# Performance work log

Hardware: AMD Instinct MI355X
Metric: run time of the kernel (lower is better)

## Reference

```python
import jax, jax.numpy as jnp
import numpy as np

B, S, D = 2, 2048, 2048
H, KVH = 32, 8
HD = D // H          # 64
Q_OUT = H * HD       # 2048
KV_OUT = KVH * HD    # 512
THETA = 10000.0


def setup_inputs() -> dict:
    key = jax.random.key(0)
    k1, k2, k3 = jax.random.split(key, 3)
    x = jax.random.normal(k1, (B, S, D), dtype=jnp.float32)
    w_qkv = jax.random.normal(k2, (Q_OUT + 2 * KV_OUT, D), dtype=jnp.float32) * 0.02
    w_out = jax.random.normal(k3, (D, D), dtype=jnp.float32) * 0.02
    gain = jnp.ones((1,), dtype=jnp.float32)
    return {"x": x, "w_qkv": w_qkv, "w_out": w_out, "gain": gain}


def _rope(t):
    # t: [b, s, h, hd]; non-interleaved (half-split) RoPE, positions = arange(s)
    s, hd = t.shape[1], t.shape[-1]
    inv_freq = 1.0 / (THETA ** (jnp.arange(0, hd // 2, dtype=jnp.float32) * 2.0 / hd))
    ang = jnp.arange(s, dtype=jnp.float32)[:, None] * inv_freq[None, :]  # [s, hd/2]
    cos = jnp.cos(ang)[None, :, None, :]
    sin = jnp.sin(ang)[None, :, None, :]
    t1, t2 = t[..., : hd // 2], t[..., hd // 2 :]
    return jnp.concatenate([t1 * cos - t2 * sin, t2 * cos + t1 * sin], axis=-1)


def _rmsnorm(t, eps=1e-6):
    # per-head-dim RMS normalization in fp32 (QK-norm)
    inv = jax.lax.rsqrt(jnp.mean(t * t, axis=-1, keepdims=True) + eps)
    return t * inv


def reference(x, w_qkv, w_out, gain):
    proj = jnp.einsum("bsd,od->bso", x, w_qkv)
    Q = proj[..., :Q_OUT].reshape(B, S, H, HD)
    K = proj[..., Q_OUT : Q_OUT + KV_OUT].reshape(B, S, KVH, HD)
    V = proj[..., Q_OUT + KV_OUT :].reshape(B, S, KVH, HD)

    Q = _rope(Q)
    K = _rope(K)

    # GQA: repeat_interleave kv heads to match query heads
    rep = H // KVH
    K = jnp.repeat(K, rep, axis=2)  # [b, s, H, hd]
    V = jnp.repeat(V, rep, axis=2)

    # value residual path (disabled): alpha1=1, alpha2=0, scale=1 -> V * rsqrt(1 + 1e-8)
    V = V * jax.lax.rsqrt(jnp.float32(1.0 + 1e-8))

    # QK-RMSNorm with learnable scalar gain on q
    Qn = _rmsnorm(Q) * gain
    Kn = _rmsnorm(K)

    scale = 1.0 / jnp.sqrt(jnp.float32(HD))
    scores = jnp.einsum("bqhd,bkhd->bhqk", Qn, Kn) * scale  # [b, H, S, S]
    causal = jnp.tril(jnp.ones((S, S), dtype=bool))
    scores = jnp.where(causal[None, None], scores, jnp.float32(-1e30))
    p = jax.nn.softmax(scores, axis=-1)
    attn = jnp.einsum("bhqk,bkhd->bqhd", p, V)  # [b, S, H, hd]

    # rearrange '(h b) seq hd -> b seq (h hd)': head index is outer in feature dim
    attn_cat = attn.transpose(0, 1, 2, 3).reshape(B, S, H * HD)
    attn_out = jnp.einsum("bsd,od->bso", attn_cat, w_out)

    # module returns (attn_out, V) with V in (h*b, seq, hd) layout
    V_flat = V.transpose(2, 0, 1, 3).reshape(H * B, S, HD)
    return attn_out, V_flat
```

## Files before the change

### kernel.cpp

```cpp
#include <hip/hip_runtime.h>
#include <hip/hip_bf16.h>
#include <cstdint>
#include <cstddef>

#define B_ 2
#define S_ 2048
#define D_ 2048
#define H_ 32
#define KVH_ 8
#define HD_ 64
#define PROJN 3072

typedef unsigned short u16;
typedef unsigned int u32;
typedef __attribute__((ext_vector_type(8))) short short8;
typedef __attribute__((ext_vector_type(4))) short short4v;
typedef __attribute__((ext_vector_type(4))) float f32x4;

__device__ __forceinline__ u16 f2bf(float f) {
  __hip_bfloat16 h = __float2bfloat16(f);
  return *reinterpret_cast<u16*>(&h);
}

__device__ __forceinline__ float fast_exp2(float x) {
  float r;
  asm("v_exp_f32 %0, %1" : "=v"(r) : "v"(x));
  return r;
}

__device__ __forceinline__ u32 pack2bf(float lo, float hi) {
  u32 a = __float_as_uint(lo) + 0x8000u;
  u32 b = __float_as_uint(hi) + 0x8000u;
  return __builtin_amdgcn_perm(b, a, 0x07060302);
}

#define GLDS16(g, l)                                                           \
  __builtin_amdgcn_global_load_lds(                                            \
      (const __attribute__((address_space(1))) void*)(g),                      \
      (__attribute__((address_space(3))) void*)(l), 16, 0, 0)

__global__ __launch_bounds__(256) void pack_bf16(const float* __restrict__ in,
                                                 u16* __restrict__ out, int n) {
  int i = (blockIdx.x * 256 + threadIdx.x) * 8;
  if (i >= n) return;
  const float4* p = reinterpret_cast<const float4*>(in + i);
  float4 a = p[0], b = p[1];
  union { short8 v; u16 u[8]; } r;
  r.u[0] = f2bf(a.x); r.u[1] = f2bf(a.y); r.u[2] = f2bf(a.z); r.u[3] = f2bf(a.w);
  r.u[4] = f2bf(b.x); r.u[5] = f2bf(b.y); r.u[6] = f2bf(b.z); r.u[7] = f2bf(b.w);
  *reinterpret_cast<short8*>(out + i) = r.v;
}

__global__ __launch_bounds__(256) void rope_tabT(float* __restrict__ tct,
                                                 float* __restrict__ tst) {
  int i = blockIdx.x * 256 + threadIdx.x;
  int j = i >> 11, s = i & 2047;
  float e = (float)(2 * j) / 64.0f;
  float inv_freq = 1.0f / powf(10000.0f, e);
  float ang = (float)s * inv_freq;
  tct[i] = cosf(ang);
  tst[i] = sinf(ang);
}

__global__ __launch_bounds__(512) void gemm_bt(const u16* __restrict__ A,
                                               const u16* __restrict__ Bw,
                                               float* __restrict__ C, int M,
                                               int N, int K) {
  __shared__ u16 As[128 * 64];
  __shared__ u16 Bs[128 * 64];
  const int tid = threadIdx.x;
  const int lane = tid & 63;
  const int wave = tid >> 6;
  const int ntile = N >> 7;
  const int m0 = (blockIdx.x / ntile) << 7;
  const int n0 = (blockIdx.x % ntile) << 7;
  const int wr = (wave >> 1) << 5;
  const int wc = (wave & 1) << 6;
  const int arow = lane & 15;
  const int kgrp = lane >> 4;

  const f32x4 zero4 = {0.f, 0.f, 0.f, 0.f};
  f32x4 acc[2][4];
#pragma unroll
  for (int m = 0; m < 2; m++)
#pragma unroll
    for (int n = 0; n < 4; n++) acc[m][n] = zero4;

  int srow[2], sslot[2];
#pragma unroll
  for (int i = 0; i < 2; i++) {
    int c = i * 512 + tid;
    srow[i] = c >> 3;
    sslot[i] = (c & 7) ^ (srow[i] & 7);
  }

  auto stage = [&](int kt) {
    const int k0 = kt << 6;
#pragma unroll
    for (int i = 0; i < 2; i++) {
      const u16* ga = A + (size_t)(m0 + srow[i]) * K + k0 + sslot[i] * 8;
      GLDS16(ga, As + (i * 512 + tid) * 8);
    }
#pragma unroll
    for (int i = 0; i < 2; i++) {
      const u16* gb = Bw + (size_t)(n0 + srow[i]) * K + k0 + sslot[i] * 8;
      GLDS16(gb, Bs + (i * 512 + tid) * 8);
    }
  };

  const int KT = K >> 6;
  stage(0);
  for (int kt = 0;; kt++) {
    __syncthreads();
#pragma unroll
    for (int ks = 0; ks < 2; ks++) {
      const int sd = ks * 4 + kgrp;
      short8 a[2], b[4];
#pragma unroll
      for (int m = 0; m < 2; m++) {
        int r = wr + m * 16 + arow;
        a[m] = *reinterpret_cast<const short8*>(As + r * 64 + ((sd ^ (r & 7)) << 3));
      }
#pragma unroll
      for (int n = 0; n < 4; n++) {
        int r = wc + n * 16 + arow;
        b[n] = *reinterpret_cast<const short8*>(Bs + r * 64 + ((sd ^ (r & 7)) << 3));
      }
#pragma unroll
      for (int m = 0; m < 2; m++)
#pragma unroll
        for (int n = 0; n < 4; n++)
          acc[m][n] = __builtin_amdgcn_mfma_f32_16x16x32_bf16(a[m], b[n], acc[m][n], 0, 0, 0);
    }
    if (kt + 1 == KT) break;
    __syncthreads();
    stage(kt + 1);
  }

  const int crow = kgrp * 4;
#pragma unroll
  for (int m = 0; m < 2; m++) {
#pragma unroll
    for (int n = 0; n < 4; n++) {
      float* cp = C + (size_t)(m0 + wr + m * 16 + crow) * N + n0 + wc + n * 16 + arow;
#pragma unroll
      for (int r = 0; r < 4; r++) cp[(size_t)r * N] = acc[m][n][r];
    }
  }
}

__global__ __launch_bounds__(512) void gemm_qkv(
    const u16* __restrict__ A, const u16* __restrict__ Bw,
    const float* __restrict__ tct, const float* __restrict__ tst,
    const float* __restrict__ gain, float* __restrict__ projV,
    u16* __restrict__ Qn, u16* __restrict__ Kn) {
  __shared__ u16 As[128 * 64];
  __shared__ u16 Bs[128 * 64];
  const int tid = threadIdx.x;
  const int lane = tid & 63;
  const int wave = tid >> 6;
  const int ntile = PROJN >> 7;
  const int m0 = (blockIdx.x / ntile) << 7;
  const int n0 = (blockIdx.x % ntile) << 7;
  const int wr = (wave >> 1) << 5;
  const int wc = (wave & 1) << 6;
  const int ql = lane & 15;
  const int g = lane >> 4;
  const int K = 2048;

  const f32x4 zero4 = {0.f, 0.f, 0.f, 0.f};
  f32x4 acc[2][4];
#pragma unroll
  for (int m = 0; m < 2; m++)
#pragma unroll
    for (int n = 0; n < 4; n++) acc[m][n] = zero4;

  int srow[2], sslot[2];
#pragma unroll
  for (int i = 0; i < 2; i++) {
    int c = i * 512 + tid;
    srow[i] = c >> 3;
    sslot[i] = (c & 7) ^ (srow[i] & 7);
  }

  auto stage = [&](int kt) {
    const int k0 = kt << 6;
#pragma unroll
    for (int i = 0; i < 2; i++) {
      const u16* ga = A + (size_t)(m0 + srow[i]) * K + k0 + sslot[i] * 8;
      GLDS16(ga, As + (i * 512 + tid) * 8);
    }
#pragma unroll
    for (int i = 0; i < 2; i++) {
      const u16* gb = Bw + (size_t)(n0 + srow[i]) * K + k0 + sslot[i] * 8;
      GLDS16(gb, Bs + (i * 512 + tid) * 8);
    }
  };

  stage(0);
  for (int kt = 0;; kt++) {
    __syncthreads();
#pragma unroll
    for (int ks = 0; ks < 2; ks++) {
      const int sd = ks * 4 + g;
      short8 a[2], b[4];
#pragma unroll
      for (int m = 0; m < 2; m++) {
        int r = wr + m * 16 + ql;
        a[m] = *reinterpret_cast<const short8*>(As + r * 64 + ((sd ^ (r & 7)) << 3));
      }
#pragma unroll
      for (int n = 0; n < 4; n++) {
        int r = wc + n * 16 + ql;
        b[n] = *reinterpret_cast<const short8*>(Bs + r * 64 + ((sd ^ (r & 7)) << 3));
      }
#pragma unroll
      for (int m = 0; m < 2; m++)
#pragma unroll
        for (int n = 0; n < 4; n++)
          acc[m][n] = __builtin_amdgcn_mfma_f32_16x16x32_bf16(a[m], b[n], acc[m][n], 0, 0, 0);
    }
    if (kt + 1 == 32) break;
    __syncthreads();
    stage(kt + 1);
  }

  const int hslice = (n0 + wc) >> 6;
  const int browbase = m0 + wr + 4 * g;
  const int bb = (m0 + wr) >> 11;

  if (hslice >= 40) {
    float* dstV = projV + (size_t)browbase * 512 + (hslice - 40) * 64;
#pragma unroll
    for (int m = 0; m < 2; m++)
#pragma unroll
      for (int n = 0; n < 4; n++) {
        float* dp = dstV + (size_t)(16 * m) * 512 + n * 16 + ql;
#pragma unroll
        for (int r = 0; r < 4; r++) dp[(size_t)r * 512] = acc[m][n][r];
      }
    return;
  }

  const bool isQ = (hslice < 32);
  const float scale = isQ ? gain[0] * 0.18033688011112042f : 1.0f;
  u16* outp = isQ ? Qn + ((size_t)(bb * H_ + hslice)) * S_ * HD_
                  : Kn + ((size_t)(bb * KVH_ + (hslice - 32))) * S_ * HD_;
  const int jj0 = ql, jj1 = 16 + ql;

#pragma unroll
  for (int m = 0; m < 2; m++) {
    const int sb = (browbase + 16 * m) & (S_ - 1);
    float c0a[4], c1a[4], s0a[4], s1a[4];
    *reinterpret_cast<float4*>(c0a) = *reinterpret_cast<const float4*>(&tct[jj0 * 2048 + sb]);
    *reinterpret_cast<float4*>(c1a) = *reinterpret_cast<const float4*>(&tct[jj1 * 2048 + sb]);
    *reinterpret_cast<float4*>(s0a) = *reinterpret_cast<const float4*>(&tst[jj0 * 2048 + sb]);
    *reinterpret_cast<float4*>(s1a) = *reinterpret_cast<const float4*>(&tst[jj1 * 2048 + sb]);
    float o[4][4], iv[4];
#pragma unroll
    for (int r = 0; r < 4; r++) {
      const float a0 = acc[m][0][r], a1 = acc[m][1][r];
      const float a2 = acc[m][2][r], a3 = acc[m][3][r];
      const float l0 = a0 * c0a[r] - a2 * s0a[r];
      const float l1 = a1 * c1a[r] - a3 * s1a[r];
      const float h0 = a2 * c0a[r] + a0 * s0a[r];
      const float h1 = a3 * c1a[r] + a1 * s1a[r];
      o[0][r] = l0; o[1][r] = l1; o[2][r] = h0; o[3][r] = h1;
      float sr = (l0 * l0 + l1 * l1) + (h0 * h0 + h1 * h1);
      sr += __shfl_xor(sr, 1);
      sr += __shfl_xor(sr, 2);
      sr += __shfl_xor(sr, 4);
      sr += __shfl_xor(sr, 8);
      iv[r] = rsqrtf(sr * (1.0f / 64.0f) + 1e-6f) * scale;
    }
#pragma unroll
    for (int n = 0; n < 4; n++) {
      const int d = n * 16 + ql;
#pragma unroll
      for (int r = 0; r < 4; r++)
        outp[(size_t)(sb + r) * HD_ + d] = f2bf(o[n][r] * iv[r]);
    }
  }
}

__global__ __launch_bounds__(256) void vtrans(const float* __restrict__ projV,
                                              u16* __restrict__ Vt,
                                              float* __restrict__ Vout) {
  __shared__ float tile[64][65];
  const int bid = blockIdx.x;
  const int st = bid & 31;
  const int s0 = st << 6;
  const int kvh = (bid >> 5) & 7;
  const int b = bid >> 8;
  const int t = threadIdx.x;
  const int sr = t >> 2;
  const int d0 = (t & 3) << 4;
  const float* src = projV + ((size_t)(b * S_ + s0 + sr)) * 512 + kvh * 64 + d0;
  float v[16];
#pragma unroll
  for (int i = 0; i < 16; i += 4) {
    float4 x = *reinterpret_cast<const float4*>(src + i);
    v[i] = x.x; v[i + 1] = x.y; v[i + 2] = x.z; v[i + 3] = x.w;
  }
#pragma unroll
  for (int hh = 0; hh < 4; hh++) {
    int hq = kvh * 4 + hh;
    float* dst = Vout + (((size_t)(hq * B_ + b)) * S_ + s0 + sr) * HD_ + d0;
#pragma unroll
    for (int i = 0; i < 16; i += 4)
      *reinterpret_cast<float4*>(dst + i) = make_float4(v[i], v[i + 1], v[i + 2], v[i + 3]);
  }
#pragma unroll
  for (int i = 0; i < 16; i++) tile[sr][d0 + i] = v[i];
  __syncthreads();
  const int d = t >> 2;
  const int sc = (t & 3) << 4;
  union { short8 v8; u16 u[8]; } o0, o1;
#pragma unroll
  for (int i = 0; i < 8; i++) o0.u[i] = f2bf(tile[sc + i][d]);
#pragma unroll
  for (int i = 0; i < 8; i++) o1.u[i] = f2bf(tile[sc + 8 + i][d]);
  u16* dst = Vt + (((size_t)(b * KVH_ + kvh)) * HD_ + d) * S_ + s0 + sc;
  *reinterpret_cast<short8*>(dst) = o0.v8;
  *reinterpret_cast<short8*>(dst + 8) = o1.v8;
}

__global__ __launch_bounds__(256, 2) void attn_fwd(const u16* __restrict__ Qn,
                                                   const u16* __restrict__ Kn,
                                                   const u16* __restrict__ Vt,
                                                   u16* __restrict__ Aout) {
  __shared__ u16 Ks[2][64 * 64];
  __shared__ u16 Vs[2][64 * 64];
  __shared__ u16 Ps[4][1024];
  const int bid = blockIdx.x;
  const int grp = bid & 15;
  const int i = bid >> 4;
  const int qt = 63 - i;
  const int b = grp >> 3;
  const int kvh = grp & 7;
  const int q0 = qt << 5;
  const int JT = (qt >> 1) + 1;
  const int tid = threadIdx.x;
  const int lane = tid & 63;
  const int wave = tid >> 6;
  const int h = kvh * 4 + wave;
  const int ql = lane & 15;
  const int g = lane >> 4;

  short8 qa[2][2];
  int rowq[2];
#pragma unroll
  for (int f = 0; f < 2; f++) {
    rowq[f] = q0 + 16 * f + ql;
    const u16* qb = Qn + (((size_t)(b * H_ + h)) * S_ + rowq[f]) * HD_;
    qa[f][0] = *reinterpret_cast<const short8*>(qb + g * 8);
    qa[f][1] = *reinterpret_cast<const short8*>(qb + 32 + g * 8);
  }

  const f32x4 zero4 = {0.f, 0.f, 0.f, 0.f};
  f32x4 oacc[4][2];
#pragma unroll
  for (int dn = 0; dn < 4; dn++)
#pragma unroll
    for (int f = 0; f < 2; f++) oacc[dn][f] = zero4;
  float psum[2] = {0.f, 0.f};

  const u16* kg = Kn + ((size_t)(b * KVH_ + kvh)) * S_ * HD_;
  const u16* vg = Vt + ((size_t)(b * KVH_ + kvh)) * HD_ * S_;

  const int c0 = tid, c1 = 256 + tid;
  const int r0 = c0 >> 3, sl0 = (c0 & 7) ^ (r0 & 7);
  const int r1 = c1 >> 3, sl1 = (c1 & 7) ^ (r1 & 7);
  const int xsw2 = (ql & 7) << 2;

  auto stage = [&](int jt, int buf) {
    const int j0 = jt << 6;
    GLDS16(kg + (size_t)(j0 + r0) * HD_ + sl0 * 8, Ks[buf] + c0 * 8);
    GLDS16(kg + (size_t)(j0 + r1) * HD_ + sl1 * 8, Ks[buf] + c1 * 8);
    GLDS16(vg + (size_t)r0 * S_ + j0 + sl0 * 8, Vs[buf] + c0 * 8);
    GLDS16(vg + (size_t)r1 * S_ + j0 + sl1 * 8, Vs[buf] + c1 * 8);
  };

  stage(0, 0);
  __syncthreads();
  int cur = 0;
  for (int jt = 0; jt < JT; jt++) {
    if (jt + 1 < JT) stage(jt + 1, cur ^ 1);
    const int j0 = jt << 6;
    const u16* ksb = Ks[cur];
    const u16* vsb = Vs[cur];
    const bool diag = (jt == JT - 1);

    f32x4 sc[4][2];
#pragma unroll
    for (int n = 0; n < 4; n++)
#pragma unroll
      for (int f = 0; f < 2; f++) sc[n][f] = zero4;
    __builtin_amdgcn_s_setprio(1);
#pragma unroll
    for (int ks = 0; ks < 2; ks++) {
      const int sd = ks * 4 + g;
#pragma unroll
      for (int n = 0; n < 4; n++) {
        const int r = n * 16 + ql;
        short8 kf = *reinterpret_cast<const short8*>(ksb + r * 64 + ((sd ^ (r & 7)) << 3));
        sc[n][0] = __builtin_amdgcn_mfma_f32_16x16x32_bf16(kf, qa[0][ks], sc[n][0], 0, 0, 0);
        sc[n][1] = __builtin_amdgcn_mfma_f32_16x16x32_bf16(kf, qa[1][ks], sc[n][1], 0, 0, 0);
      }
    }
    __builtin_amdgcn_s_setprio(0);

    short8 pa[2][2];
#pragma unroll
    for (int f = 0; f < 2; f++) {
      float pv[4][4];
#pragma unroll
      for (int n = 0; n < 4; n++)
#pragma unroll
        for (int r = 0; r < 4; r++)
          pv[n][r] = fast_exp2(sc[n][f][r]);
      if (diag) {
#pragma unroll
        for (int n = 0; n < 4; n++)
#pragma unroll
          for (int r = 0; r < 4; r++)
            if ((j0 + n * 16 + 4 * g + r) > rowq[f]) pv[n][r] = 0.f;
      }
      u32* pw32 = reinterpret_cast<u32*>(Ps[wave]);
#pragma unroll
      for (int n = 0; n < 4; n++) {
        psum[f] += (pv[n][0] + pv[n][1]) + (pv[n][2] + pv[n][3]);
        const int idx = ql * 32 + (((n << 3) + (g << 1)) ^ xsw2);
        pw32[idx] = pack2bf(pv[n][0], pv[n][1]);
        pw32[idx + 1] = pack2bf(pv[n][2], pv[n][3]);
      }
#pragma unroll
      for (int ks = 0; ks < 2; ks++)
        pa[f][ks] = *reinterpret_cast<const short8*>(
            Ps[wave] + ql * 64 + ((32 * ks + 8 * g) ^ (xsw2 << 1)));
    }

    __builtin_amdgcn_s_setprio(1);
#pragma unroll
    for (int ks = 0; ks < 2; ks++) {
      const int sd = ks * 4 + g;
#pragma unroll
      for (int dn = 0; dn < 4; dn++) {
        const int vr = dn * 16 + ql;
        short8 vf = *reinterpret_cast<const short8*>(vsb + vr * 64 + ((sd ^ (vr & 7)) << 3));
        oacc[dn][0] = __builtin_amdgcn_mfma_f32_16x16x32_bf16(vf, pa[0][ks], oacc[dn][0], 0, 0, 0);
        oacc[dn][1] = __builtin_amdgcn_mfma_f32_16x16x32_bf16(vf, pa[1][ks], oacc[dn][1], 0, 0, 0);
      }
    }
    __builtin_amdgcn_s_setprio(0);

    __syncthreads();
    cur ^= 1;
  }

#pragma unroll
  for (int f = 0; f < 2; f++) {
    float s = psum[f];
    s += __shfl_xor(s, 16);
    s += __shfl_xor(s, 32);
    const float il = 1.0f / s;
#pragma unroll
    for (int dn = 0; dn < 4; dn++) {
      union { short4v v; u16 uu[4]; } o;
#pragma unroll
      for (int r = 0; r < 4; r++) o.uu[r] = f2bf(oacc[dn][f][r] * il);
      u16* dst = Aout + ((size_t)b * S_ + rowq[f]) * D_ + h * HD_ + dn * 16 + 4 * g;
      *reinterpret_cast<short4v*>(dst) = o.v;
    }
  }
}

extern "C" void kernel_launch(void* const* d_in, const int* in_sizes, int n_in,
                              void* d_out, int out_size, void* d_ws,
                              size_t ws_size, hipStream_t stream) {
  const float* x = (const float*)d_in[0];
  const float* wqkv = (const float*)d_in[1];
  const float* wout = (const float*)d_in[2];
  const float* gain = (const float*)d_in[3];

  float* out_attn = (float*)d_out;
  float* out_vflat = out_attn + (size_t)B_ * S_ * D_;

  uint8_t* w = (uint8_t*)d_ws;
  u16* xb      = (u16*)(w);
  u16* wqkvb   = (u16*)(w + 16777216);
  u16* woutb   = (u16*)(w + 29360128);
  float* projV = (float*)(w + 37748736);
  u16* Qn      = (u16*)(w + 46137344);
  u16* Kn      = (u16*)(w + 62914560);
  u16* Vt      = (u16*)(w + 67108864);
  u16* attnb   = (u16*)(w + 71303168);
  float* tct   = (float*)(w + 88080384);
  float* tst   = (float*)(w + 88342528);

  pack_bf16<<<4096, 256, 0, stream>>>(x, xb, B_ * S_ * D_);
  pack_bf16<<<3072, 256, 0, stream>>>(wqkv, wqkvb, PROJN * D_);
  pack_bf16<<<2048, 256, 0, stream>>>(wout, woutb, D_ * D_);
  rope_tabT<<<256, 256, 0, stream>>>(tct, tst);

  gemm_qkv<<<(4096 / 128) * (3072 / 128), 512, 0, stream>>>(
      xb, wqkvb, tct, tst, gain, projV, Qn, Kn);
  vtrans<<<B_ * KVH_ * (S_ / 64), 256, 0, stream>>>(projV, Vt, out_vflat);
  attn_fwd<<<B_ * KVH_ * (S_ / 32), 256, 0, stream>>>(Qn, Kn, Vt, attnb);
  gemm_bt<<<(4096 / 128) * (2048 / 128), 512, 0, stream>>>(attnb, woutb,
                                                           out_attn, 4096,
                                                           2048, 2048);
}
```

Measured before the change: 210.1 us.

## Double-buffer LDS in both GEMMs and merge three pack kernels into one

Both bf16 GEMM kernels now use two LDS buffers and prefetch two k-tiles ahead. Explicit vmcnt waits plus raw s_barrier let the global-to-LDS loads for tile k+2 overlap the MFMA work on tile k, instead of serialising load and compute with a sync each iteration. The three fp32-to-bf16 pack launches are merged into a single launch to cut launch overhead. LDS use per block doubles to 64 KB, which may lower occupancy, and the hand-written vmcnt counts depend on each thread issuing exactly four loads per stage.

```diff
diff --git a/kernel.cpp b/kernel.cpp
--- a/kernel.cpp
+++ b/kernel.cpp
@@ -39,10 +39,20 @@
       (const __attribute__((address_space(1))) void*)(g),                      \
       (__attribute__((address_space(3))) void*)(l), 16, 0, 0)
 
-__global__ __launch_bounds__(256) void pack_bf16(const float* __restrict__ in,
-                                                 u16* __restrict__ out, int n) {
-  int i = (blockIdx.x * 256 + threadIdx.x) * 8;
-  if (i >= n) return;
+__global__ __launch_bounds__(256) void pack3(const float* __restrict__ x,
+                                             const float* __restrict__ wqkv,
+                                             const float* __restrict__ wout,
+                                             u16* __restrict__ xb,
+                                             u16* __restrict__ wqkvb,
+                                             u16* __restrict__ woutb) {
+  const int bid = blockIdx.x;
+  const float* in;
+  u16* out;
+  int base;
+  if (bid < 4096) { in = x; out = xb; base = bid; }
+  else if (bid < 7168) { in = wqkv; out = wqkvb; base = bid - 4096; }
+  else { in = wout; out = woutb; base = bid - 7168; }
+  const int i = (base * 256 + threadIdx.x) * 8;
   const float4* p = reinterpret_cast<const float4*>(in + i);
   float4 a = p[0], b = p[1];
   union { short8 v; u16 u[8]; } r;
@@ -66,8 +76,8 @@
                                                const u16* __restrict__ Bw,
                                                float* __restrict__ C, int M,
                                                int N, int K) {
-  __shared__ u16 As[128 * 64];
-  __shared__ u16 Bs[128 * 64];
+  __shared__ u16 As[2][128 * 64];
+  __shared__ u16 Bs[2][128 * 64];
   const int tid = threadIdx.x;
   const int lane = tid & 63;
   const int wave = tid >> 6;
@@ -94,24 +104,31 @@
     sslot[i] = (c & 7) ^ (srow[i] & 7);
   }
 
-  auto stage = [&](int kt) {
+  auto stage = [&](int kt, int buf) {
     const int k0 = kt << 6;
 #pragma unroll
     for (int i = 0; i < 2; i++) {
       const u16* ga = A + (size_t)(m0 + srow[i]) * K + k0 + sslot[i] * 8;
-      GLDS16(ga, As + (i * 512 + tid) * 8);
+      GLDS16(ga, As[buf] + (i * 512 + tid) * 8);
     }
 #pragma unroll
     for (int i = 0; i < 2; i++) {
       const u16* gb = Bw + (size_t)(n0 + srow[i]) * K + k0 + sslot[i] * 8;
-      GLDS16(gb, Bs + (i * 512 + tid) * 8);
+      GLDS16(gb, Bs[buf] + (i * 512 + tid) * 8);
     }
   };
 
   const int KT = K >> 6;
-  stage(0);
-  for (int kt = 0;; kt++) {
-    __syncthreads();
+  stage(0, 0);
+  stage(1, 1);
+  int cur = 0;
+  for (int kt = 0; kt < KT; kt++) {
+    if (kt + 1 < KT) asm volatile("s_waitcnt vmcnt(4)" ::: "memory");
+    else             asm volatile("s_waitcnt vmcnt(0)" ::: "memory");
+    __builtin_amdgcn_s_barrier();
+    __builtin_amdgcn_sched_barrier(0);
+    const u16* Asb = As[cur];
+    const u16* Bsb = Bs[cur];
 #pragma unroll
     for (int ks = 0; ks < 2; ks++) {
       const int sd = ks * 4 + kgrp;
@@ -119,12 +136,12 @@
 #pragma unroll
       for (int m = 0; m < 2; m++) {
         int r = wr + m * 16 + arow;
-        a[m] = *reinterpret_cast<const short8*>(As + r * 64 + ((sd ^ (r & 7)) << 3));
+        a[m] = *reinterpret_cast<const short8*>(Asb + r * 64 + ((sd ^ (r & 7)) << 3));
       }
 #pragma unroll
       for (int n = 0; n < 4; n++) {
         int r = wc + n * 16 + arow;
-        b[n] = *reinterpret_cast<const short8*>(Bs + r * 64 + ((sd ^ (r & 7)) << 3));
+        b[n] = *reinterpret_cast<const short8*>(Bsb + r * 64 + ((sd ^ (r & 7)) << 3));
       }
 #pragma unroll
       for (int m = 0; m < 2; m++)
@@ -132,9 +149,10 @@
         for (int n = 0; n < 4; n++)
           acc[m][n] = __builtin_amdgcn_mfma_f32_16x16x32_bf16(a[m], b[n], acc[m][n], 0, 0, 0);
     }
-    if (kt + 1 == KT) break;
-    __syncthreads();
-    stage(kt + 1);
+    __builtin_amdgcn_sched_barrier(0);
+    __builtin_amdgcn_s_barrier();
+    if (kt + 2 < KT) stage(kt + 2, cur);
+    cur ^= 1;
   }
 
   const int crow = kgrp * 4;
@@ -154,8 +172,8 @@
     const float* __restrict__ tct, const float* __restrict__ tst,
     const float* __restrict__ gain, float* __restrict__ projV,
     u16* __restrict__ Qn, u16* __restrict__ Kn) {
-  __shared__ u16 As[128 * 64];
-  __shared__ u16 Bs[128 * 64];
+  __shared__ u16 As[2][128 * 64];
+  __shared__ u16 Bs[2][128 * 64];
   const int tid = threadIdx.x;
   const int lane = tid & 63;
   const int wave = tid >> 6;
@@ -183,23 +201,31 @@
     sslot[i] = (c & 7) ^ (srow[i] & 7);
   }
 
-  auto stage = [&](int kt) {
+  auto stage = [&](int kt, int buf) {
     const int k0 = kt << 6;
 #pragma unroll
     for (int i = 0; i < 2; i++) {
       const u16* ga = A + (size_t)(m0 + srow[i]) * K + k0 + sslot[i] * 8;
-      GLDS16(ga, As + (i * 512 + tid) * 8);
+      GLDS16(ga, As[buf] + (i * 512 + tid) * 8);
     }
 #pragma unroll
     for (int i = 0; i < 2; i++) {
       const u16* gb = Bw + (size_t)(n0 + srow[i]) * K + k0 + sslot[i] * 8;
-      GLDS16(gb, Bs + (i * 512 + tid) * 8);
+      GLDS16(gb, Bs[buf] + (i * 512 + tid) * 8);
     }
   };
 
-  stage(0);
-  for (int kt = 0;; kt++) {
-    __syncthreads();
+  const int KT = 32;
+  stage(0, 0);
+  stage(1, 1);
+  int cur = 0;
+  for (int kt = 0; kt < KT; kt++) {
+    if (kt + 1 < KT) asm volatile("s_waitcnt vmcnt(4)" ::: "memory");
+    else             asm volatile("s_waitcnt vmcnt(0)" ::: "memory");
+    __builtin_amdgcn_s_barrier();
+    __builtin_amdgcn_sched_barrier(0);
+    const u16* Asb = As[cur];
+    const u16* Bsb = Bs[cur];
 #pragma unroll
     for (int ks = 0; ks < 2; ks++) {
       const int sd = ks * 4 + g;
@@ -207,12 +233,12 @@
 #pragma unroll
       for (int m = 0; m < 2; m++) {
         int r = wr + m * 16 + ql;
-        a[m] = *reinterpret_cast<const short8*>(As + r * 64 + ((sd ^ (r & 7)) << 3));
+        a[m] = *reinterpret_cast<const short8*>(Asb + r * 64 + ((sd ^ (r & 7)) << 3));
       }
 #pragma unroll
       for (int n = 0; n < 4; n++) {
         int r = wc + n * 16 + ql;
-        b[n] = *reinterpret_cast<const short8*>(Bs + r * 64 + ((sd ^ (r & 7)) << 3));
+        b[n] = *reinterpret_cast<const short8*>(Bsb + r * 64 + ((sd ^ (r & 7)) << 3));
       }
 #pragma unroll
       for (int m = 0; m < 2; m++)
@@ -220,9 +246,10 @@
         for (int n = 0; n < 4; n++)
           acc[m][n] = __builtin_amdgcn_mfma_f32_16x16x32_bf16(a[m], b[n], acc[m][n], 0, 0, 0);
     }
-    if (kt + 1 == 32) break;
-    __syncthreads();
-    stage(kt + 1);
+    __builtin_amdgcn_sched_barrier(0);
+    __builtin_amdgcn_s_barrier();
+    if (kt + 2 < KT) stage(kt + 2, cur);
+    cur ^= 1;
   }
 
   const int hslice = (n0 + wc) >> 6;
@@ -498,9 +525,7 @@
   float* tct   = (float*)(w + 88080384);
   float* tst   = (float*)(w + 88342528);
 
-  pack_bf16<<<4096, 256, 0, stream>>>(x, xb, B_ * S_ * D_);
-  pack_bf16<<<3072, 256, 0, stream>>>(wqkv, wqkvb, PROJN * D_);
-  pack_bf16<<<2048, 256, 0, stream>>>(wout, woutb, D_ * D_);
+  pack3<<<9216, 256, 0, stream>>>(x, wqkv, wout, xb, wqkvb, woutb);
   rope_tabT<<<256, 256, 0, stream>>>(tct, tst);
 
   gemm_qkv<<<(4096 / 128) * (3072 / 128), 512, 0, stream>>>(
```

Result: faster. 201.2 us (-4.2%).
